# Kernel tuning notes

Measured on AMD Instinct MI355X. Metric: run time of the kernel, lower is better.

Reference implementation:

```python
import jax, jax.numpy as jnp
import numpy as np

D = 64          # feature dim
H_POS = 64      # pos_mlp hidden
H_ATTN = 4 * D  # attn_mlp hidden
B, N = 1, 1024


def setup_inputs() -> dict:
    key = jax.random.key(0)
    ks = jax.random.split(key, 12)
    s = lambda fan_in: 1.0 / np.sqrt(fan_in)
    return {
        "x": jax.random.normal(ks[0], (B, N, D), jnp.float32),
        "pos": jax.random.normal(ks[1], (B, N, 2), jnp.float32),
        "Wq": jax.random.normal(ks[2], (D, D), jnp.float32) * s(D),
        "Wk": jax.random.normal(ks[3], (D, D), jnp.float32) * s(D),
        "Wv": jax.random.normal(ks[4], (D, D), jnp.float32) * s(D),
        "pW1": jax.random.normal(ks[5], (2, H_POS), jnp.float32) * s(2),
        "pb1": jnp.zeros((H_POS,), jnp.float32),
        "pW2": jax.random.normal(ks[6], (H_POS, D), jnp.float32) * s(H_POS),
        "pb2": jnp.zeros((D,), jnp.float32),
        "aW1": jax.random.normal(ks[7], (D, H_ATTN), jnp.float32) * s(D),
        "ab1": jnp.zeros((H_ATTN,), jnp.float32),
        "aW2": jax.random.normal(ks[8], (H_ATTN, D), jnp.float32) * s(H_ATTN),
        "ab2": jnp.zeros((D,), jnp.float32),
    }


def reference(x, pos, Wq, Wk, Wv, pW1, pb1, pW2, pb2, aW1, ab1, aW2, ab2):
    # projections: [b, n, d]
    q = x @ Wq
    k = x @ Wk
    v = x @ Wv
    # pairwise relative positions: [b, i, j, 2]
    rel_pos = pos[:, :, None, :] - pos[:, None, :, :]
    # pos MLP: [b, i, j, d]
    rpe = jax.nn.relu(rel_pos @ pW1 + pb1) @ pW2 + pb2
    # pairwise q - k: [b, i, j, d]
    qk_rel = q[:, :, None, :] - k[:, None, :, :]
    # values broadcast over i, plus positional embedding: [b, i, j, d]
    vv = v[:, None, :, :] + rpe
    # attention MLP on (qk_rel + rpe): [b, i, j, d]
    sim = jax.nn.relu((qk_rel + rpe) @ aW1 + ab1) @ aW2 + ab2
    # softmax over j (axis=-2), per-channel
    attn = jax.nn.softmax(sim, axis=-2)
    # weighted aggregation: [b, i, d]
    agg = jnp.einsum('bijd,bijd->bid', attn, vv)
    return agg
```

## Files before the change

kernel.cpp:

```cpp
#include <hip/hip_runtime.h>


typedef float f32x4 __attribute__((ext_vector_type(4)));
typedef int   i32x8 __attribute__((ext_vector_type(8)));
using sh8 = __attribute__((ext_vector_type(8))) short;

static constexpr int NPTS = 1024;

#if __has_builtin(__builtin_amdgcn_exp2f)
#define EXP2(x) __builtin_amdgcn_exp2f(x)
#else
#define EXP2(x) exp2f(x)
#endif

static constexpr size_t BEXT_OFF = 0;
static constexpr size_t AW2F_OFF = 65536;
static constexpr size_t PW2F_OFF = 98304;
static constexpr size_t CARR_OFF = 106496;
static constexpr size_t AI_OFF   = 107520;
static constexpr size_t QI_OFF   = 369664;
static constexpr size_t VPT_OFF  = 631808;
static constexpr size_t AJ_OFF   = 893952;
static constexpr size_t KN_OFF   = 1025024;

__device__ __forceinline__ unsigned short f2b_rne(float f) {
    unsigned u = __float_as_uint(f);
    u += 0x7fffu + ((u >> 16) & 1u);
    return (unsigned short)(u >> 16);
}
__device__ __forceinline__ unsigned pk2(float lo, float hi) {
    return __builtin_amdgcn_perm(__float_as_uint(hi), __float_as_uint(lo), 0x07060302);
}
__device__ __forceinline__ float b2f(unsigned short s) {
    return __uint_as_float(((unsigned)s) << 16);
}
__device__ __forceinline__ unsigned char f2fp8(float v) {
    return (unsigned char)(__builtin_amdgcn_cvt_pk_fp8_f32(v, 0.f, 0, false) & 0xff);
}
__device__ __forceinline__ unsigned pk4fp8(float a, float b, float c, float d) {
    int r = __builtin_amdgcn_cvt_pk_fp8_f32(a, b, 0, false);
    r = __builtin_amdgcn_cvt_pk_fp8_f32(c, d, r, true);
    return (unsigned)r;
}
__device__ __forceinline__ i32x8 ld32B(const void* p) {
    const uint4 a = ((const uint4*)p)[0];
    const uint4 b = ((const uint4*)p)[1];
    i32x8 r;
    r[0] = a.x; r[1] = a.y; r[2] = a.z; r[3] = a.w;
    r[4] = b.x; r[5] = b.y; r[6] = b.z; r[7] = b.w;
    return r;
}

__global__ void prep_all(const float* __restrict__ x, const float* __restrict__ pos,
                         const float* __restrict__ Wq, const float* __restrict__ Wk,
                         const float* __restrict__ Wv, const float* __restrict__ pW1,
                         const float* __restrict__ pb1, const float* __restrict__ pW2,
                         const float* __restrict__ pb2, const float* __restrict__ aW1,
                         const float* __restrict__ ab1, const float* __restrict__ aW2,
                         unsigned short* __restrict__ bextf, unsigned char* __restrict__ aw2f8,
                         unsigned short* __restrict__ pw2f, float* __restrict__ cArr,
                         float* __restrict__ qI, unsigned short* __restrict__ kN,
                         float* __restrict__ vPT, float* __restrict__ aI,
                         unsigned short* __restrict__ aJ)
{
    const int b = blockIdx.x;
    if (b < 209) {
        const int idx = b * 256 + threadIdx.x;
        if (idx < 32768) {
            const int k = idx >> 8, t = idx & 255;
            float val;
            if (k < 64) {
                float s = 0.f;
                for (int d = 0; d < 64; ++d) s = fmaf(pW2[k * 64 + d], aW1[d * 256 + t], s);
                val = s;
            } else {
                val = aW1[(k - 64) * 256 + t];
            }
            const int kc = k >> 5, kl = k & 31, qq = kl >> 3, e = kl & 7;
            const int ntg = t >> 4, tl = t & 15;
            bextf[(((size_t)(kc * 16 + ntg) * 64) + (qq * 16 + tl)) * 8 + e] = f2b_rne(val);
        } else if (idx < 49152) {
            const int r = idx - 32768;
            const int e = r & 31, lane = (r >> 5) & 63, wsl = (r >> 11) & 3, kb = r >> 13;
            const int q = lane >> 4, dl = lane & 15;
            const int kp = kb * 128 + q * 32 + e;
            const int t = 64 * (kp >> 6) + 16 * (kp & 3) + ((kp >> 2) & 15);
            const int d = 16 * wsl + dl;
            aw2f8[r] = f2fp8(aW2[t * 64 + d] * 1.4426950408889634f);
        } else if (idx < 53248) {
            const int r = idx - 49152;
            const int k = r >> 6, d = r & 63;
            const int kc = k >> 5, kl = k & 31, qq = kl >> 3, e = kl & 7;
            const int nt = d >> 4, dl = d & 15;
            pw2f[(((size_t)(kc * 4 + nt) * 64) + (qq * 16 + dl)) * 8 + e] = f2b_rne(pW2[k * 64 + d]);
        } else if (idx < 53504) {
            const int t = idx - 53248;
            float s = ab1[t];
            for (int d = 0; d < 64; ++d) s = fmaf(pb2[d], aW1[d * 256 + t], s);
            cArr[t] = s;
        }
    } else {
        const int t = threadIdx.x, sub = t >> 6, d = t & 63;
        const int i = (b - 209) * 4 + sub;
        __shared__ float xs[4][64];
        xs[sub][d] = x[i * 64 + d];
        __syncthreads();
        float q = 0.f, k = 0.f, v = 0.f;
        for (int e = 0; e < 64; ++e) {
            const float xe = xs[sub][e];
            q = fmaf(xe, Wq[e * 64 + d], q);
            k = fmaf(xe, Wk[e * 64 + d], k);
            v = fmaf(xe, Wv[e * 64 + d], v);
        }
        const float a = pos[i * 2] * pW1[d] + pos[i * 2 + 1] * pW1[64 + d];
        qI[i * 64 + d] = q;
        kN[i * 64 + d] = f2b_rne(-k);
        vPT[d * NPTS + i] = v + pb2[d];
        aI[i * 64 + d] = a + pb1[d];
        aJ[i * 64 + d] = f2b_rne(a);
    }
}

__global__ __launch_bounds__(256, 2) void ptl_main(
    const float* __restrict__ aI, const float* __restrict__ qI,
    const unsigned short* __restrict__ aJ, const unsigned short* __restrict__ kN,
    const float* __restrict__ vPT,
    const unsigned short* __restrict__ bextf, const unsigned char* __restrict__ aw2f8,
    const unsigned short* __restrict__ pw2f, const float* __restrict__ cArr,
    float* __restrict__ out)
{
    const int i    = blockIdx.x;
    const int tid  = threadIdx.x;
    const int w    = tid >> 6;
    const int lane = tid & 63;
    const int m    = lane & 15;
    const int q    = lane >> 4;

    __shared__ __align__(16) uint4 AfL[2][2][4][64];
    __shared__ __align__(16) unsigned char Hs[2][2][16 * 272];

    sh8 Bf[16];
#pragma unroll
    for (int kc = 0; kc < 4; ++kc)
#pragma unroll
        for (int nt = 0; nt < 4; ++nt)
            Bf[kc * 4 + nt] = *(const sh8*)(bextf + ((size_t)((kc * 16 + 4 * w + nt) * 64 + lane)) * 8);
    i32x8 W2f[2];
#pragma unroll
    for (int kb = 0; kb < 2; ++kb)
        W2f[kb] = ld32B(aw2f8 + ((size_t)((kb * 4 + w) * 64 + lane)) * 32);
    sh8 P2f[2];
#pragma unroll
    for (int kc = 0; kc < 2; ++kc)
        P2f[kc] = *(const sh8*)(pw2f + ((size_t)((kc * 4 + w) * 64 + lane)) * 8);

    float creg[4];
#pragma unroll
    for (int nt = 0; nt < 4; ++nt) creg[nt] = cArr[64 * w + 16 * nt + m];

    const int  half   = w & 1;
    const bool isRelu = (w < 2);
    const unsigned short* bsrc  = (isRelu ? aJ : kN) + m * 64 + half * 32 + q * 8;
    const float*          ibase = (isRelu ? aI : qI) + i * 64 + half * 32 + q * 8;
    float iv[8];
    *(float4*)(iv)     = *(const float4*)(ibase);
    *(float4*)(iv + 4) = *(const float4*)(ibase + 4);

#pragma unroll
    for (int s = 0; s < 2; ++s) {
        const sh8 raw = *(const sh8*)(bsrc + (size_t)(16 * s) * 64);
        float t[8];
#pragma unroll
        for (int e = 0; e < 8; ++e)
            t[e] = isRelu ? fmaxf(iv[e] - b2f((unsigned short)raw[e]), 0.f)
                          : iv[e] + b2f((unsigned short)raw[e]);
        uint4 pk;
        pk.x = pk2(t[0], t[1]); pk.y = pk2(t[2], t[3]);
        pk.z = pk2(t[4], t[5]); pk.w = pk2(t[6], t[7]);
        AfL[0][s][w][lane] = pk;
    }
    __syncthreads();

    float num = 0.f, den = 0.f;
    const f32x4 z4 = {0.f, 0.f, 0.f, 0.f};
    f32x4 aRp0 = z4, aRp1 = z4;
    const float* vbase = vPT + (size_t)(16 * w + m) * NPTS;

    for (int n = 0; n < 32; ++n) {
        const int pb = n & 1, nb = pb ^ 1;
        const int j0 = n << 5;

        sh8 raw0, raw1;
        if (n < 31) {
            raw0 = *(const sh8*)(bsrc + (size_t)(j0 + 32) * 64);
            raw1 = *(const sh8*)(bsrc + (size_t)(j0 + 48) * 64);
        }
        const float4 vj0 = *(const float4*)(vbase + j0 + 4 * q);
        const float4 vj1 = *(const float4*)(vbase + j0 + 16 + 4 * q);

        const sh8 A00 = *(const sh8*)&AfL[pb][0][0][lane];
        const sh8 A01 = *(const sh8*)&AfL[pb][0][1][lane];
        const sh8 A02 = *(const sh8*)&AfL[pb][0][2][lane];
        const sh8 A03 = *(const sh8*)&AfL[pb][0][3][lane];
        {
            f32x4 acc[4];
#pragma unroll
            for (int nt = 0; nt < 4; ++nt) {
                const f32x4 cv = {creg[nt], creg[nt], creg[nt], creg[nt]};
                acc[nt] = __builtin_amdgcn_mfma_f32_16x16x32_bf16(A00, Bf[0 * 4 + nt], cv, 0, 0, 0);
                acc[nt] = __builtin_amdgcn_mfma_f32_16x16x32_bf16(A01, Bf[1 * 4 + nt], acc[nt], 0, 0, 0);
                acc[nt] = __builtin_amdgcn_mfma_f32_16x16x32_bf16(A02, Bf[2 * 4 + nt], acc[nt], 0, 0, 0);
                acc[nt] = __builtin_amdgcn_mfma_f32_16x16x32_bf16(A03, Bf[3 * 4 + nt], acc[nt], 0, 0, 0);
            }
            unsigned char* hw = Hs[pb][0] + (4 * q) * 272 + 64 * w + 4 * m;
#pragma unroll
            for (int r = 0; r < 4; ++r)
                *(unsigned*)(hw + r * 272) = pk4fp8(fmaxf(acc[0][r], 0.f), fmaxf(acc[1][r], 0.f),
                                                   fmaxf(acc[2][r], 0.f), fmaxf(acc[3][r], 0.f));
        }

        i32x8 h00, h01, h10, h11;
        if (n) {
            h00 = ld32B(Hs[nb][0] + m * 272 + 0   + 32 * q);
            h01 = ld32B(Hs[nb][0] + m * 272 + 128 + 32 * q);
            h10 = ld32B(Hs[nb][1] + m * 272 + 0   + 32 * q);
            h11 = ld32B(Hs[nb][1] + m * 272 + 128 + 32 * q);
        }

        const sh8 A10 = *(const sh8*)&AfL[pb][1][0][lane];
        const sh8 A11 = *(const sh8*)&AfL[pb][1][1][lane];
        const sh8 A12 = *(const sh8*)&AfL[pb][1][2][lane];
        const sh8 A13 = *(const sh8*)&AfL[pb][1][3][lane];
        {
            f32x4 acc[4];
#pragma unroll
            for (int nt = 0; nt < 4; ++nt) {
                const f32x4 cv = {creg[nt], creg[nt], creg[nt], creg[nt]};
                acc[nt] = __builtin_amdgcn_mfma_f32_16x16x32_bf16(A10, Bf[0 * 4 + nt], cv, 0, 0, 0);
                acc[nt] = __builtin_amdgcn_mfma_f32_16x16x32_bf16(A11, Bf[1 * 4 + nt], acc[nt], 0, 0, 0);
                acc[nt] = __builtin_amdgcn_mfma_f32_16x16x32_bf16(A12, Bf[2 * 4 + nt], acc[nt], 0, 0, 0);
                acc[nt] = __builtin_amdgcn_mfma_f32_16x16x32_bf16(A13, Bf[3 * 4 + nt], acc[nt], 0, 0, 0);
            }
            unsigned char* hw = Hs[pb][1] + (4 * q) * 272 + 64 * w + 4 * m;
#pragma unroll
            for (int r = 0; r < 4; ++r)
                *(unsigned*)(hw + r * 272) = pk4fp8(fmaxf(acc[0][r], 0.f), fmaxf(acc[1][r], 0.f),
                                                   fmaxf(acc[2][r], 0.f), fmaxf(acc[3][r], 0.f));
        }

        if (n) {
            f32x4 aS0 = z4, aS1 = z4;
            aS0 = __builtin_amdgcn_mfma_scale_f32_16x16x128_f8f6f4(
                h00, W2f[0], aS0, 0, 0, 0, 127, 0, 127);
            aS0 = __builtin_amdgcn_mfma_scale_f32_16x16x128_f8f6f4(
                h01, W2f[1], aS0, 0, 0, 0, 127, 0, 127);
            aS1 = __builtin_amdgcn_mfma_scale_f32_16x16x128_f8f6f4(
                h10, W2f[0], aS1, 0, 0, 0, 127, 0, 127);
            aS1 = __builtin_amdgcn_mfma_scale_f32_16x16x128_f8f6f4(
                h11, W2f[1], aS1, 0, 0, 0, 127, 0, 127);
#pragma unroll
            for (int r = 0; r < 4; ++r) {
                const float e0 = EXP2(aS0[r]);
                num = fmaf(e0, aRp0[r], num);
                den += e0;
                const float e1 = EXP2(aS1[r]);
                num = fmaf(e1, aRp1[r], num);
                den += e1;
            }
        }

        const f32x4 vc0 = {vj0.x, vj0.y, vj0.z, vj0.w};
        const f32x4 vc1 = {vj1.x, vj1.y, vj1.z, vj1.w};
        f32x4 aR0 = __builtin_amdgcn_mfma_f32_16x16x32_bf16(A00, P2f[0], vc0, 0, 0, 0);
        aR0 = __builtin_amdgcn_mfma_f32_16x16x32_bf16(A01, P2f[1], aR0, 0, 0, 0);
        f32x4 aR1 = __builtin_amdgcn_mfma_f32_16x16x32_bf16(A10, P2f[0], vc1, 0, 0, 0);
        aR1 = __builtin_amdgcn_mfma_f32_16x16x32_bf16(A11, P2f[1], aR1, 0, 0, 0);
        aRp0 = aR0;
        aRp1 = aR1;

        if (n < 31) {
#pragma unroll
            for (int s = 0; s < 2; ++s) {
                const sh8 raw = s ? raw1 : raw0;
                float t[8];
#pragma unroll
                for (int e = 0; e < 8; ++e)
                    t[e] = isRelu ? fmaxf(iv[e] - b2f((unsigned short)raw[e]), 0.f)
                                  : iv[e] + b2f((unsigned short)raw[e]);
                uint4 pk;
                pk.x = pk2(t[0], t[1]); pk.y = pk2(t[2], t[3]);
                pk.z = pk2(t[4], t[5]); pk.w = pk2(t[6], t[7]);
                AfL[nb][s][w][lane] = pk;
            }
        }

        __syncthreads();
    }

    {
        f32x4 aS0 = z4, aS1 = z4;
        const i32x8 h00 = ld32B(Hs[1][0] + m * 272 + 0   + 32 * q);
        const i32x8 h01 = ld32B(Hs[1][0] + m * 272 + 128 + 32 * q);
        const i32x8 h10 = ld32B(Hs[1][1] + m * 272 + 0   + 32 * q);
        const i32x8 h11 = ld32B(Hs[1][1] + m * 272 + 128 + 32 * q);
        aS0 = __builtin_amdgcn_mfma_scale_f32_16x16x128_f8f6f4(
            h00, W2f[0], aS0, 0, 0, 0, 127, 0, 127);
        aS0 = __builtin_amdgcn_mfma_scale_f32_16x16x128_f8f6f4(
            h01, W2f[1], aS0, 0, 0, 0, 127, 0, 127);
        aS1 = __builtin_amdgcn_mfma_scale_f32_16x16x128_f8f6f4(
            h10, W2f[0], aS1, 0, 0, 0, 127, 0, 127);
        aS1 = __builtin_amdgcn_mfma_scale_f32_16x16x128_f8f6f4(
            h11, W2f[1], aS1, 0, 0, 0, 127, 0, 127);
#pragma unroll
        for (int r = 0; r < 4; ++r) {
            const float e0 = EXP2(aS0[r]);
            num = fmaf(e0, aRp0[r], num);
            den += e0;
            const float e1 = EXP2(aS1[r]);
            num = fmaf(e1, aRp1[r], num);
            den += e1;
        }
    }

    num += __shfl_xor(num, 16);
    num += __shfl_xor(num, 32);
    den += __shfl_xor(den, 16);
    den += __shfl_xor(den, 32);
    if (q == 0) out[i * 64 + 16 * w + m] = num / den;
}

extern "C" void kernel_launch(void* const* d_in, const int* in_sizes, int n_in,
                              void* d_out, int out_size, void* d_ws, size_t ws_size,
                              hipStream_t stream) {
    const float* x   = (const float*)d_in[0];
    const float* pos = (const float*)d_in[1];
    const float* Wq  = (const float*)d_in[2];
    const float* Wk  = (const float*)d_in[3];
    const float* Wv  = (const float*)d_in[4];
    const float* pW1 = (const float*)d_in[5];
    const float* pb1 = (const float*)d_in[6];
    const float* pW2 = (const float*)d_in[7];
    const float* pb2 = (const float*)d_in[8];
    const float* aW1 = (const float*)d_in[9];
    const float* ab1 = (const float*)d_in[10];
    const float* aW2 = (const float*)d_in[11];

    char* ws = (char*)d_ws;
    unsigned short* bextf = (unsigned short*)(ws + BEXT_OFF);
    unsigned char*  aw2f8 = (unsigned char*)(ws + AW2F_OFF);
    unsigned short* pw2f  = (unsigned short*)(ws + PW2F_OFF);
    float*          cArr  = (float*)(ws + CARR_OFF);
    float*          aIa   = (float*)(ws + AI_OFF);
    float*          qIa   = (float*)(ws + QI_OFF);
    float*          vPTa  = (float*)(ws + VPT_OFF);
    unsigned short* aJa   = (unsigned short*)(ws + AJ_OFF);
    unsigned short* kNa   = (unsigned short*)(ws + KN_OFF);

    prep_all<<<465, 256, 0, stream>>>(x, pos, Wq, Wk, Wv, pW1, pb1, pW2, pb2, aW1, ab1, aW2,
                                      bextf, aw2f8, pw2f, cArr, qIa, kNa, vPTa, aIa, aJa);
    ptl_main<<<NPTS, 256, 0, stream>>>(aIa, qIa, aJa, kNa, vPTa, bextf, aw2f8, pw2f, cArr,
                                       (float*)d_out);
}
```

Baseline: 180.8 us.

## Precompute q·aW1 and k·aW1 per point to halve main-loop MFMA K dimension

Splits the first attention-MLP layer so the query and key projections through aW1 are computed once per point in the prep kernel (qa per row, transposed knat per column) instead of per pair inside the main loop. The main kernel now runs only the positional-embedding half of the bf16 MFMA chain and adds the key term from global memory and the query term into the bias. This removes half the pairwise matrix work and the q/k fragment staging, but adds per-iteration global loads of the key term and a larger prep launch.

```diff
diff --git a/kernel.cpp b/kernel.cpp
--- a/kernel.cpp
+++ b/kernel.cpp
@@ -15,13 +15,13 @@
 
 static constexpr size_t BEXT_OFF = 0;
 static constexpr size_t AW2F_OFF = 65536;
-static constexpr size_t PW2F_OFF = 98304;
-static constexpr size_t CARR_OFF = 106496;
-static constexpr size_t AI_OFF   = 107520;
-static constexpr size_t QI_OFF   = 369664;
-static constexpr size_t VPT_OFF  = 631808;
-static constexpr size_t AJ_OFF   = 893952;
-static constexpr size_t KN_OFF   = 1025024;
+static constexpr size_t PW2F_OFF = 81920;
+static constexpr size_t CARR_OFF = 90112;
+static constexpr size_t AI_OFF   = 91136;
+static constexpr size_t AJ_OFF   = 353280;
+static constexpr size_t VPT_OFF  = 484352;
+static constexpr size_t QA_OFF   = 746496;
+static constexpr size_t KNAT_OFF = 1795072;
 
 __device__ __forceinline__ unsigned short f2b_rne(float f) {
     unsigned u = __float_as_uint(f);
@@ -59,74 +59,92 @@
                          const float* __restrict__ ab1, const float* __restrict__ aW2,
                          unsigned short* __restrict__ bextf, unsigned char* __restrict__ aw2f8,
                          unsigned short* __restrict__ pw2f, float* __restrict__ cArr,
-                         float* __restrict__ qI, unsigned short* __restrict__ kN,
                          float* __restrict__ vPT, float* __restrict__ aI,
-                         unsigned short* __restrict__ aJ)
+                         unsigned short* __restrict__ aJ, float* __restrict__ qa,
+                         float* __restrict__ knat)
 {
+    __shared__ float s1[4][64];
+    __shared__ float s2[4][64];
     const int b = blockIdx.x;
-    if (b < 209) {
+    if (b < 64) {
         const int idx = b * 256 + threadIdx.x;
-        if (idx < 32768) {
-            const int k = idx >> 8, t = idx & 255;
-            float val;
-            if (k < 64) {
-                float s = 0.f;
-                for (int d = 0; d < 64; ++d) s = fmaf(pW2[k * 64 + d], aW1[d * 256 + t], s);
-                val = s;
-            } else {
-                val = aW1[(k - 64) * 256 + t];
-            }
-            const int kc = k >> 5, kl = k & 31, qq = kl >> 3, e = kl & 7;
-            const int ntg = t >> 4, tl = t & 15;
-            bextf[(((size_t)(kc * 16 + ntg) * 64) + (qq * 16 + tl)) * 8 + e] = f2b_rne(val);
-        } else if (idx < 49152) {
-            const int r = idx - 32768;
-            const int e = r & 31, lane = (r >> 5) & 63, wsl = (r >> 11) & 3, kb = r >> 13;
-            const int q = lane >> 4, dl = lane & 15;
-            const int kp = kb * 128 + q * 32 + e;
-            const int t = 64 * (kp >> 6) + 16 * (kp & 3) + ((kp >> 2) & 15);
-            const int d = 16 * wsl + dl;
-            aw2f8[r] = f2fp8(aW2[t * 64 + d] * 1.4426950408889634f);
-        } else if (idx < 53248) {
-            const int r = idx - 49152;
-            const int k = r >> 6, d = r & 63;
-            const int kc = k >> 5, kl = k & 31, qq = kl >> 3, e = kl & 7;
-            const int nt = d >> 4, dl = d & 15;
-            pw2f[(((size_t)(kc * 4 + nt) * 64) + (qq * 16 + dl)) * 8 + e] = f2b_rne(pW2[k * 64 + d]);
-        } else if (idx < 53504) {
-            const int t = idx - 53248;
-            float s = ab1[t];
-            for (int d = 0; d < 64; ++d) s = fmaf(pb2[d], aW1[d * 256 + t], s);
-            cArr[t] = s;
-        }
-    } else {
+        const int k = idx >> 8, t = idx & 255;
+        float s = 0.f;
+        for (int d = 0; d < 64; ++d) s = fmaf(pW2[k * 64 + d], aW1[d * 256 + t], s);
+        const int kc = k >> 5, kl = k & 31, qq = kl >> 3, e = kl & 7;
+        const int ntg = t >> 4, tl = t & 15;
+        bextf[(((size_t)(kc * 16 + ntg) * 64) + (qq * 16 + tl)) * 8 + e] = f2b_rne(s);
+    } else if (b < 128) {
+        const int r = (b - 64) * 256 + threadIdx.x;
+        const int e = r & 31, lane = (r >> 5) & 63, wsl = (r >> 11) & 3, kb = r >> 13;
+        const int q = lane >> 4, dl = lane & 15;
+        const int kp = kb * 128 + q * 32 + e;
+        const int t = 64 * (kp >> 6) + 16 * (kp & 3) + ((kp >> 2) & 15);
+        const int d = 16 * wsl + dl;
+        aw2f8[r] = f2fp8(aW2[t * 64 + d] * 1.4426950408889634f);
+    } else if (b < 144) {
+        const int r = (b - 128) * 256 + threadIdx.x;
+        const int k = r >> 6, d = r & 63;
+        const int kc = k >> 5, kl = k & 31, qq = kl >> 3, e = kl & 7;
+        const int nt = d >> 4, dl = d & 15;
+        pw2f[(((size_t)(kc * 4 + nt) * 64) + (qq * 16 + dl)) * 8 + e] = f2b_rne(pW2[k * 64 + d]);
+    } else if (b == 144) {
+        const int t = threadIdx.x;
+        float s = ab1[t];
+        for (int d = 0; d < 64; ++d) s = fmaf(pb2[d], aW1[d * 256 + t], s);
+        cArr[t] = s;
+    } else if (b < 401) {
         const int t = threadIdx.x, sub = t >> 6, d = t & 63;
-        const int i = (b - 209) * 4 + sub;
-        __shared__ float xs[4][64];
-        xs[sub][d] = x[i * 64 + d];
-        __syncthreads();
-        float q = 0.f, k = 0.f, v = 0.f;
-        for (int e = 0; e < 64; ++e) {
-            const float xe = xs[sub][e];
-            q = fmaf(xe, Wq[e * 64 + d], q);
-            k = fmaf(xe, Wk[e * 64 + d], k);
-            v = fmaf(xe, Wv[e * 64 + d], v);
-        }
+        const int i = (b - 145) * 4 + sub;
+        s1[sub][d] = x[i * 64 + d];
+        __syncthreads();
+        float v = 0.f;
+        for (int e = 0; e < 64; ++e) v = fmaf(s1[sub][e], Wv[e * 64 + d], v);
         const float a = pos[i * 2] * pW1[d] + pos[i * 2 + 1] * pW1[64 + d];
-        qI[i * 64 + d] = q;
-        kN[i * 64 + d] = f2b_rne(-k);
         vPT[d * NPTS + i] = v + pb2[d];
         aI[i * 64 + d] = a + pb1[d];
         aJ[i * 64 + d] = f2b_rne(a);
+    } else if (b < 1425) {
+        const int i = b - 401, t = threadIdx.x;
+        if (t < 64) s1[0][t] = x[i * 64 + t];
+        __syncthreads();
+        if (t < 64) {
+            float s = 0.f;
+            for (int e = 0; e < 64; ++e) s = fmaf(s1[0][e], Wq[e * 64 + t], s);
+            s2[0][t] = s;
+        }
+        __syncthreads();
+        float s = 0.f;
+        for (int d = 0; d < 64; ++d) s = fmaf(s2[0][d], aW1[d * 256 + t], s);
+        qa[(size_t)i * 256 + t] = s;
+    } else {
+        const int j0 = (b - 1425) * 4, t = threadIdx.x;
+        const int jj = t >> 6, d = t & 63;
+        s1[jj][d] = x[(j0 + jj) * 64 + d];
+        __syncthreads();
+        float s = 0.f;
+        for (int e = 0; e < 64; ++e) s = fmaf(s1[jj][e], Wk[e * 64 + d], s);
+        s2[jj][d] = s;
+        __syncthreads();
+        float r0 = 0.f, r1 = 0.f, r2 = 0.f, r3 = 0.f;
+        for (int d2 = 0; d2 < 64; ++d2) {
+            const float wv = aW1[d2 * 256 + t];
+            r0 = fmaf(s2[0][d2], wv, r0);
+            r1 = fmaf(s2[1][d2], wv, r1);
+            r2 = fmaf(s2[2][d2], wv, r2);
+            r3 = fmaf(s2[3][d2], wv, r3);
+        }
+        float4 o = {-r0, -r1, -r2, -r3};
+        *(float4*)(knat + (size_t)t * NPTS + j0) = o;
     }
 }
 
 __global__ __launch_bounds__(256, 2) void ptl_main(
-    const float* __restrict__ aI, const float* __restrict__ qI,
-    const unsigned short* __restrict__ aJ, const unsigned short* __restrict__ kN,
+    const float* __restrict__ aI, const unsigned short* __restrict__ aJ,
     const float* __restrict__ vPT,
     const unsigned short* __restrict__ bextf, const unsigned char* __restrict__ aw2f8,
     const unsigned short* __restrict__ pw2f, const float* __restrict__ cArr,
+    const float* __restrict__ qa, const float* __restrict__ knat,
     float* __restrict__ out)
 {
     const int i    = blockIdx.x;
@@ -136,12 +154,12 @@
     const int m    = lane & 15;
     const int q    = lane >> 4;
 
-    __shared__ __align__(16) uint4 AfL[2][2][4][64];
+    __shared__ __align__(16) uint4 AfL[2][2][2][64];
     __shared__ __align__(16) unsigned char Hs[2][2][16 * 272];
 
-    sh8 Bf[16];
-#pragma unroll
-    for (int kc = 0; kc < 4; ++kc)
+    sh8 Bf[8];
+#pragma unroll
+    for (int kc = 0; kc < 2; ++kc)
 #pragma unroll
         for (int nt = 0; nt < 4; ++nt)
             Bf[kc * 4 + nt] = *(const sh8*)(bextf + ((size_t)((kc * 16 + 4 * w + nt) * 64 + lane)) * 8);
@@ -156,52 +174,53 @@
 
     float creg[4];
 #pragma unroll
-    for (int nt = 0; nt < 4; ++nt) creg[nt] = cArr[64 * w + 16 * nt + m];
-
-    const int  half   = w & 1;
-    const bool isRelu = (w < 2);
-    const unsigned short* bsrc  = (isRelu ? aJ : kN) + m * 64 + half * 32 + q * 8;
-    const float*          ibase = (isRelu ? aI : qI) + i * 64 + half * 32 + q * 8;
+    for (int nt = 0; nt < 4; ++nt)
+        creg[nt] = cArr[64 * w + 16 * nt + m] + qa[(size_t)i * 256 + 64 * w + 16 * nt + m];
+
+    const int s_ = w >> 1, h_ = w & 1;
+    const unsigned short* bsrc  = aJ + m * 64 + h_ * 32 + q * 8;
+    const float*          ibase = aI + i * 64 + h_ * 32 + q * 8;
     float iv[8];
     *(float4*)(iv)     = *(const float4*)(ibase);
     *(float4*)(iv + 4) = *(const float4*)(ibase + 4);
 
-#pragma unroll
-    for (int s = 0; s < 2; ++s) {
-        const sh8 raw = *(const sh8*)(bsrc + (size_t)(16 * s) * 64);
+    {
+        const sh8 raw = *(const sh8*)(bsrc + (size_t)(16 * s_) * 64);
         float t[8];
 #pragma unroll
         for (int e = 0; e < 8; ++e)
-            t[e] = isRelu ? fmaxf(iv[e] - b2f((unsigned short)raw[e]), 0.f)
-                          : iv[e] + b2f((unsigned short)raw[e]);
+            t[e] = fmaxf(iv[e] - b2f((unsigned short)raw[e]), 0.f);
         uint4 pk;
         pk.x = pk2(t[0], t[1]); pk.y = pk2(t[2], t[3]);
         pk.z = pk2(t[4], t[5]); pk.w = pk2(t[6], t[7]);
-        AfL[0][s][w][lane] = pk;
+        AfL[0][s_][h_][lane] = pk;
     }
     __syncthreads();
 
     float num = 0.f, den = 0.f;
     const f32x4 z4 = {0.f, 0.f, 0.f, 0.f};
     f32x4 aRp0 = z4, aRp1 = z4;
-    const float* vbase = vPT + (size_t)(16 * w + m) * NPTS;
+    const float* vbase  = vPT + (size_t)(16 * w + m) * NPTS;
+    const float* knbase = knat + (size_t)(64 * w + m) * NPTS;
 
     for (int n = 0; n < 32; ++n) {
         const int pb = n & 1, nb = pb ^ 1;
         const int j0 = n << 5;
 
-        sh8 raw0, raw1;
-        if (n < 31) {
-            raw0 = *(const sh8*)(bsrc + (size_t)(j0 + 32) * 64);
-            raw1 = *(const sh8*)(bsrc + (size_t)(j0 + 48) * 64);
-        }
+        sh8 rawN;
+        if (n < 31) rawN = *(const sh8*)(bsrc + (size_t)(j0 + 32 + 16 * s_) * 64);
         const float4 vj0 = *(const float4*)(vbase + j0 + 4 * q);
         const float4 vj1 = *(const float4*)(vbase + j0 + 16 + 4 * q);
+        f32x4 ka0[4];
+#pragma unroll
+        for (int nt = 0; nt < 4; ++nt)
+            ka0[nt] = *(const f32x4*)(knbase + (size_t)nt * 16 * NPTS + j0 + 4 * q);
 
         const sh8 A00 = *(const sh8*)&AfL[pb][0][0][lane];
         const sh8 A01 = *(const sh8*)&AfL[pb][0][1][lane];
-        const sh8 A02 = *(const sh8*)&AfL[pb][0][2][lane];
-        const sh8 A03 = *(const sh8*)&AfL[pb][0][3][lane];
+        const sh8 A10 = *(const sh8*)&AfL[pb][1][0][lane];
+        const sh8 A11 = *(const sh8*)&AfL[pb][1][1][lane];
+
         {
             f32x4 acc[4];
 #pragma unroll
@@ -209,8 +228,7 @@
                 const f32x4 cv = {creg[nt], creg[nt], creg[nt], creg[nt]};
                 acc[nt] = __builtin_amdgcn_mfma_f32_16x16x32_bf16(A00, Bf[0 * 4 + nt], cv, 0, 0, 0);
                 acc[nt] = __builtin_amdgcn_mfma_f32_16x16x32_bf16(A01, Bf[1 * 4 + nt], acc[nt], 0, 0, 0);
-                acc[nt] = __builtin_amdgcn_mfma_f32_16x16x32_bf16(A02, Bf[2 * 4 + nt], acc[nt], 0, 0, 0);
-                acc[nt] = __builtin_amdgcn_mfma_f32_16x16x32_bf16(A03, Bf[3 * 4 + nt], acc[nt], 0, 0, 0);
+                acc[nt] = acc[nt] + ka0[nt];
             }
             unsigned char* hw = Hs[pb][0] + (4 * q) * 272 + 64 * w + 4 * m;
 #pragma unroll
@@ -218,6 +236,11 @@
                 *(unsigned*)(hw + r * 272) = pk4fp8(fmaxf(acc[0][r], 0.f), fmaxf(acc[1][r], 0.f),
                                                    fmaxf(acc[2][r], 0.f), fmaxf(acc[3][r], 0.f));
         }
+
+        f32x4 ka1[4];
+#pragma unroll
+        for (int nt = 0; nt < 4; ++nt)
+            ka1[nt] = *(const f32x4*)(knbase + (size_t)nt * 16 * NPTS + j0 + 16 + 4 * q);
 
         i32x8 h00, h01, h10, h11;
         if (n) {
@@ -227,10 +250,6 @@
             h11 = ld32B(Hs[nb][1] + m * 272 + 128 + 32 * q);
         }
 
-        const sh8 A10 = *(const sh8*)&AfL[pb][1][0][lane];
-        const sh8 A11 = *(const sh8*)&AfL[pb][1][1][lane];
-        const sh8 A12 = *(const sh8*)&AfL[pb][1][2][lane];
-        const sh8 A13 = *(const sh8*)&AfL[pb][1][3][lane];
         {
             f32x4 acc[4];
 #pragma unroll
@@ -238,8 +257,7 @@
                 const f32x4 cv = {creg[nt], creg[nt], creg[nt], creg[nt]};
                 acc[nt] = __builtin_amdgcn_mfma_f32_16x16x32_bf16(A10, Bf[0 * 4 + nt], cv, 0, 0, 0);
                 acc[nt] = __builtin_amdgcn_mfma_f32_16x16x32_bf16(A11, Bf[1 * 4 + nt], acc[nt], 0, 0, 0);
-                acc[nt] = __builtin_amdgcn_mfma_f32_16x16x32_bf16(A12, Bf[2 * 4 + nt], acc[nt], 0, 0, 0);
-                acc[nt] = __builtin_amdgcn_mfma_f32_16x16x32_bf16(A13, Bf[3 * 4 + nt], acc[nt], 0, 0, 0);
+                acc[nt] = acc[nt] + ka1[nt];
             }
             unsigned char* hw = Hs[pb][1] + (4 * q) * 272 + 64 * w + 4 * m;
 #pragma unroll
@@ -279,19 +297,14 @@
         aRp1 = aR1;
 
         if (n < 31) {
-#pragma unroll
-            for (int s = 0; s < 2; ++s) {
-                const sh8 raw = s ? raw1 : raw0;
-                float t[8];
-#pragma unroll
-                for (int e = 0; e < 8; ++e)
-                    t[e] = isRelu ? fmaxf(iv[e] - b2f((unsigned short)raw[e]), 0.f)
-                                  : iv[e] + b2f((unsigned short)raw[e]);
-                uint4 pk;
-                pk.x = pk2(t[0], t[1]); pk.y = pk2(t[2], t[3]);
-                pk.z = pk2(t[4], t[5]); pk.w = pk2(t[6], t[7]);
-                AfL[nb][s][w][lane] = pk;
-            }
+            float t[8];
+#pragma unroll
+            for (int e = 0; e < 8; ++e)
+                t[e] = fmaxf(iv[e] - b2f((unsigned short)rawN[e]), 0.f);
+            uint4 pk;
+            pk.x = pk2(t[0], t[1]); pk.y = pk2(t[2], t[3]);
+            pk.z = pk2(t[4], t[5]); pk.w = pk2(t[6], t[7]);
+            AfL[nb][s_][h_][lane] = pk;
         }
 
         __syncthreads();
@@ -351,13 +364,13 @@
     unsigned short* pw2f  = (unsigned short*)(ws + PW2F_OFF);
     float*          cArr  = (float*)(ws + CARR_OFF);
     float*          aIa   = (float*)(ws + AI_OFF);
-    float*          qIa   = (float*)(ws + QI_OFF);
+    unsigned short* aJa   = (unsigned short*)(ws + AJ_OFF);
     float*          vPTa  = (float*)(ws + VPT_OFF);
-    unsigned short* aJa   = (unsigned short*)(ws + AJ_OFF);
-    unsigned short* kNa   = (unsigned short*)(ws + KN_OFF);
-
-    prep_all<<<465, 256, 0, stream>>>(x, pos, Wq, Wk, Wv, pW1, pb1, pW2, pb2, aW1, ab1, aW2,
-                                      bextf, aw2f8, pw2f, cArr, qIa, kNa, vPTa, aIa, aJa);
-    ptl_main<<<NPTS, 256, 0, stream>>>(aIa, qIa, aJa, kNa, vPTa, bextf, aw2f8, pw2f, cArr,
+    float*          qaA   = (float*)(ws + QA_OFF);
+    float*          knatA = (float*)(ws + KNAT_OFF);
+
+    prep_all<<<1681, 256, 0, stream>>>(x, pos, Wq, Wk, Wv, pW1, pb1, pW2, pb2, aW1, ab1, aW2,
+                                       bextf, aw2f8, pw2f, cArr, vPTa, aIa, aJa, qaA, knatA);
+    ptl_main<<<NPTS, 256, 0, stream>>>(aIa, aJa, vPTa, bextf, aw2f8, pw2f, cArr, qaA, knatA,
                                        (float*)d_out);
 }
```

Result: slower. 249.9 us (+38.2%).

## Fold per-row q projection through aW1 into bias, drop per-pair q add

Applied to the files above, without the earlier changes.

The q_i contribution to the attention MLP's first layer is constant across j, so it is precomputed once per row as q_i @ aW1 in extra prep blocks and added to the per-channel bias register. Inside the main loop the k half of the A operand then becomes just the raw bf16 -k values, written straight to shared memory without the q add or repacking. Each wave now builds one 16-row slice instead of two. The cost is 1024 more prep blocks and a 1 MB qa buffer, and q@aW1 is now done in fp32 rather than rounded to bf16 through the MFMA.

```diff
diff --git a/kernel.cpp b/kernel.cpp
--- a/kernel.cpp
+++ b/kernel.cpp
@@ -18,10 +18,10 @@
 static constexpr size_t PW2F_OFF = 98304;
 static constexpr size_t CARR_OFF = 106496;
 static constexpr size_t AI_OFF   = 107520;
-static constexpr size_t QI_OFF   = 369664;
-static constexpr size_t VPT_OFF  = 631808;
-static constexpr size_t AJ_OFF   = 893952;
-static constexpr size_t KN_OFF   = 1025024;
+static constexpr size_t VPT_OFF  = 369664;
+static constexpr size_t AJ_OFF   = 631808;
+static constexpr size_t KN_OFF   = 762880;
+static constexpr size_t QA_OFF   = 893952;
 
 __device__ __forceinline__ unsigned short f2b_rne(float f) {
     unsigned u = __float_as_uint(f);
@@ -59,10 +59,12 @@
                          const float* __restrict__ ab1, const float* __restrict__ aW2,
                          unsigned short* __restrict__ bextf, unsigned char* __restrict__ aw2f8,
                          unsigned short* __restrict__ pw2f, float* __restrict__ cArr,
-                         float* __restrict__ qI, unsigned short* __restrict__ kN,
-                         float* __restrict__ vPT, float* __restrict__ aI,
-                         unsigned short* __restrict__ aJ)
+                         unsigned short* __restrict__ kN, float* __restrict__ vPT,
+                         float* __restrict__ aI, unsigned short* __restrict__ aJ,
+                         float* __restrict__ qa)
 {
+    __shared__ float s1[4][64];
+    __shared__ float s2[4][64];
     const int b = blockIdx.x;
     if (b < 209) {
         const int idx = b * 256 + threadIdx.x;
@@ -99,35 +101,44 @@
             for (int d = 0; d < 64; ++d) s = fmaf(pb2[d], aW1[d * 256 + t], s);
             cArr[t] = s;
         }
-    } else {
+    } else if (b < 465) {
         const int t = threadIdx.x, sub = t >> 6, d = t & 63;
         const int i = (b - 209) * 4 + sub;
-        __shared__ float xs[4][64];
-        xs[sub][d] = x[i * 64 + d];
+        s1[sub][d] = x[i * 64 + d];
         __syncthreads();
-        float q = 0.f, k = 0.f, v = 0.f;
+        float k = 0.f, v = 0.f;
         for (int e = 0; e < 64; ++e) {
-            const float xe = xs[sub][e];
-            q = fmaf(xe, Wq[e * 64 + d], q);
+            const float xe = s1[sub][e];
             k = fmaf(xe, Wk[e * 64 + d], k);
             v = fmaf(xe, Wv[e * 64 + d], v);
         }
         const float a = pos[i * 2] * pW1[d] + pos[i * 2 + 1] * pW1[64 + d];
-        qI[i * 64 + d] = q;
         kN[i * 64 + d] = f2b_rne(-k);
         vPT[d * NPTS + i] = v + pb2[d];
         aI[i * 64 + d] = a + pb1[d];
         aJ[i * 64 + d] = f2b_rne(a);
+    } else {
+        const int i = b - 465, t = threadIdx.x;
+        if (t < 64) s1[0][t] = x[i * 64 + t];
+        __syncthreads();
+        if (t < 64) {
+            float s = 0.f;
+            for (int e = 0; e < 64; ++e) s = fmaf(s1[0][e], Wq[e * 64 + t], s);
+            s2[0][t] = s;
+        }
+        __syncthreads();
+        float s = 0.f;
+        for (int d = 0; d < 64; ++d) s = fmaf(s2[0][d], aW1[d * 256 + t], s);
+        qa[(size_t)i * 256 + t] = s;
     }
 }
 
 __global__ __launch_bounds__(256, 2) void ptl_main(
-    const float* __restrict__ aI, const float* __restrict__ qI,
-    const unsigned short* __restrict__ aJ, const unsigned short* __restrict__ kN,
-    const float* __restrict__ vPT,
+    const float* __restrict__ aI, const unsigned short* __restrict__ aJ,
+    const unsigned short* __restrict__ kN, const float* __restrict__ vPT,
     const unsigned short* __restrict__ bextf, const unsigned char* __restrict__ aw2f8,
     const unsigned short* __restrict__ pw2f, const float* __restrict__ cArr,
-    float* __restrict__ out)
+    const float* __restrict__ qa, float* __restrict__ out)
 {
     const int i    = blockIdx.x;
     const int tid  = threadIdx.x;
@@ -156,28 +167,29 @@
 
     float creg[4];
 #pragma unroll
-    for (int nt = 0; nt < 4; ++nt) creg[nt] = cArr[64 * w + 16 * nt + m];
-
-    const int  half   = w & 1;
-    const bool isRelu = (w < 2);
-    const unsigned short* bsrc  = (isRelu ? aJ : kN) + m * 64 + half * 32 + q * 8;
-    const float*          ibase = (isRelu ? aI : qI) + i * 64 + half * 32 + q * 8;
+    for (int nt = 0; nt < 4; ++nt)
+        creg[nt] = cArr[64 * w + 16 * nt + m] + qa[(size_t)i * 256 + 64 * w + 16 * nt + m];
+
+    const int s_ = w >> 1, h_ = w & 1;
+    const unsigned short* bsrcA = aJ + m * 64 + h_ * 32 + q * 8;
+    const unsigned short* bsrcK = kN + m * 64 + h_ * 32 + q * 8;
+    const float*          ibase = aI + (size_t)i * 64 + h_ * 32 + q * 8;
     float iv[8];
     *(float4*)(iv)     = *(const float4*)(ibase);
     *(float4*)(iv + 4) = *(const float4*)(ibase + 4);
 
-#pragma unroll
-    for (int s = 0; s < 2; ++s) {
-        const sh8 raw = *(const sh8*)(bsrc + (size_t)(16 * s) * 64);
+    {
+        const sh8  rawA = *(const sh8*)(bsrcA + (size_t)(16 * s_) * 64);
+        const uint4 rawK = *(const uint4*)(bsrcK + (size_t)(16 * s_) * 64);
         float t[8];
 #pragma unroll
         for (int e = 0; e < 8; ++e)
-            t[e] = isRelu ? fmaxf(iv[e] - b2f((unsigned short)raw[e]), 0.f)
-                          : iv[e] + b2f((unsigned short)raw[e]);
+            t[e] = fmaxf(iv[e] - b2f((unsigned short)rawA[e]), 0.f);
         uint4 pk;
         pk.x = pk2(t[0], t[1]); pk.y = pk2(t[2], t[3]);
         pk.z = pk2(t[4], t[5]); pk.w = pk2(t[6], t[7]);
-        AfL[0][s][w][lane] = pk;
+        AfL[0][s_][h_][lane]     = pk;
+        AfL[0][s_][2 + h_][lane] = rawK;
     }
     __syncthreads();
 
@@ -190,10 +202,11 @@
         const int pb = n & 1, nb = pb ^ 1;
         const int j0 = n << 5;
 
-        sh8 raw0, raw1;
+        sh8  rawA;
+        uint4 rawK;
         if (n < 31) {
-            raw0 = *(const sh8*)(bsrc + (size_t)(j0 + 32) * 64);
-            raw1 = *(const sh8*)(bsrc + (size_t)(j0 + 48) * 64);
+            rawA = *(const sh8*)(bsrcA + (size_t)(j0 + 32 + 16 * s_) * 64);
+            rawK = *(const uint4*)(bsrcK + (size_t)(j0 + 32 + 16 * s_) * 64);
         }
         const float4 vj0 = *(const float4*)(vbase + j0 + 4 * q);
         const float4 vj1 = *(const float4*)(vbase + j0 + 16 + 4 * q);
@@ -279,19 +292,15 @@
         aRp1 = aR1;
 
         if (n < 31) {
-#pragma unroll
-            for (int s = 0; s < 2; ++s) {
-                const sh8 raw = s ? raw1 : raw0;
-                float t[8];
-#pragma unroll
-                for (int e = 0; e < 8; ++e)
-                    t[e] = isRelu ? fmaxf(iv[e] - b2f((unsigned short)raw[e]), 0.f)
-                                  : iv[e] + b2f((unsigned short)raw[e]);
-                uint4 pk;
-                pk.x = pk2(t[0], t[1]); pk.y = pk2(t[2], t[3]);
-                pk.z = pk2(t[4], t[5]); pk.w = pk2(t[6], t[7]);
-                AfL[nb][s][w][lane] = pk;
-            }
+            float t[8];
+#pragma unroll
+            for (int e = 0; e < 8; ++e)
+                t[e] = fmaxf(iv[e] - b2f((unsigned short)rawA[e]), 0.f);
+            uint4 pk;
+            pk.x = pk2(t[0], t[1]); pk.y = pk2(t[2], t[3]);
+            pk.z = pk2(t[4], t[5]); pk.w = pk2(t[6], t[7]);
+            AfL[nb][s_][h_][lane]     = pk;
+            AfL[nb][s_][2 + h_][lane] = rawK;
         }
 
         __syncthreads();
@@ -351,13 +360,13 @@
     unsigned short* pw2f  = (unsigned short*)(ws + PW2F_OFF);
     float*          cArr  = (float*)(ws + CARR_OFF);
     float*          aIa   = (float*)(ws + AI_OFF);
-    float*          qIa   = (float*)(ws + QI_OFF);
     float*          vPTa  = (float*)(ws + VPT_OFF);
     unsigned short* aJa   = (unsigned short*)(ws + AJ_OFF);
     unsigned short* kNa   = (unsigned short*)(ws + KN_OFF);
-
-    prep_all<<<465, 256, 0, stream>>>(x, pos, Wq, Wk, Wv, pW1, pb1, pW2, pb2, aW1, ab1, aW2,
-                                      bextf, aw2f8, pw2f, cArr, qIa, kNa, vPTa, aIa, aJa);
-    ptl_main<<<NPTS, 256, 0, stream>>>(aIa, qIa, aJa, kNa, vPTa, bextf, aw2f8, pw2f, cArr,
+    float*          qaA   = (float*)(ws + QA_OFF);
+
+    prep_all<<<1489, 256, 0, stream>>>(x, pos, Wq, Wk, Wv, pW1, pb1, pW2, pb2, aW1, ab1, aW2,
+                                       bextf, aw2f8, pw2f, cArr, kNa, vPTa, aIa, aJa, qaA);
+    ptl_main<<<NPTS, 256, 0, stream>>>(aIa, aJa, kNa, vPTa, bextf, aw2f8, pw2f, cArr, qaA,
                                        (float*)d_out);
 }
```

After: 175.1 us. 1.03x faster.
